# Kernel optimization log

Measured on AMD Instinct MI355X. Metric: run time of the kernel, lower is better.

The kernel has to match this reference:

```python
import jax, jax.numpy as jnp
import numpy as np

IN_F = 4096
OUT_F = 11008
FP_F = 256


def setup_inputs() -> dict:
    key = jax.random.key(0)
    ks = jax.random.split(key, 6)
    x = jax.random.normal(ks[0], (8, 64, IN_F), dtype=jnp.float32)
    # int8-valued quantized weight, stored as int32 for the harness
    q_weight = jax.random.randint(ks[1], (OUT_F, IN_F), -128, 128, dtype=jnp.int32)
    # per-output-column weight scale (like absmax/127), small positive
    scale_col = (jax.random.uniform(ks[2], (1, OUT_F), dtype=jnp.float32) * 0.01 + 1e-4)
    # fp16-precision outlier weight columns (kept fp32 here)
    weight_cache = jax.random.normal(ks[3], (OUT_F, FP_F), dtype=jnp.float32) * 0.02
    # outlier column indices into in_features
    ind = jnp.sort(jax.random.randint(ks[4], (FP_F,), 0, IN_F, dtype=jnp.int32))
    bias = jax.random.normal(ks[5], (OUT_F,), dtype=jnp.float32) * 0.01
    return {"x": x, "q_weight": q_weight, "scale_col": scale_col,
            "weight_cache": weight_cache, "ind": ind, "bias": bias}


def reference(x, q_weight, scale_col, weight_cache, ind, bias):
    # Flatten leading dims: (M, in_features)
    inputs = x.reshape(-1, x.shape[-1])
    # ExtractOutliersAndSetToZeros: gather outlier activation columns, zero them
    act_outliers = inputs[:, ind]                       # (M, fp)
    inputs_z = inputs.at[:, ind].set(0.0)               # (M, in)
    # FindRowScale: per-row absmax / 127, then symmetric int8 quantization
    x_scale = jnp.max(jnp.abs(inputs_z), axis=1, keepdims=True) / 127.0  # (M,1)
    x_scale = jnp.maximum(x_scale, jnp.float32(1e-8))
    q_x = jnp.clip(jnp.round(inputs_z / x_scale), -128.0, 127.0)          # int8 values
    # int8 GEMM (accumulate in fp32): (M,in) @ (in,out)
    y_int = q_x @ q_weight.T.astype(jnp.float32)
    # fp16 outlier GEMM: (M,fp) @ (fp,out)
    outliers_fp = act_outliers @ weight_cache.T
    # dequantize: row scale * col scale, add outlier contribution and bias
    y1 = y_int * x_scale * scale_col + outliers_fp + bias
    return y1.reshape(x.shape[:-1] + (q_weight.shape[0],))
```

## Files before the change

kernel.cpp:

```cpp
#include <hip/hip_runtime.h>
#include <hip/hip_fp16.h>

#define IN_F 4096
#define OUT_F 11008
#define FP_F 256
#define NROWS 512
#define BN 64

typedef int v4i __attribute__((ext_vector_type(4)));
typedef float v4f __attribute__((ext_vector_type(4)));
typedef _Float16 half8 __attribute__((ext_vector_type(8)));

__device__ __forceinline__ int pack4(v4i a) {
  return (int)((unsigned)(a[0] & 255) | ((unsigned)(a[1] & 255) << 8) |
               ((unsigned)(a[2] & 255) << 16) | ((unsigned)(a[3] & 255) << 24));
}

__global__ __launch_bounds__(256) void quant_kernel(
    const float* __restrict__ x, const int* __restrict__ ind,
    signed char* __restrict__ qx, _Float16* __restrict__ act,
    float* __restrict__ xscale)
{
  const int m = blockIdx.x;
  const int t = threadIdx.x;
  __shared__ unsigned char zm[IN_F];
  __shared__ float wmax[4];
  int* zmi = (int*)zm;
  #pragma unroll
  for (int i = 0; i < IN_F / 4 / 256; ++i) zmi[t + i * 256] = 0;
  __syncthreads();
  const int idx = ind[t];
  zm[idx] = 1;
  __syncthreads();

  const float* xr = x + (size_t)m * IN_F;
  float v[16];
  float amax = 0.f;
  const int k0 = t * 16;
  #pragma unroll
  for (int q = 0; q < 4; ++q) {
    v4f f = *(const v4f*)(xr + k0 + q * 4);
    #pragma unroll
    for (int j = 0; j < 4; ++j) {
      float mv = zm[k0 + q * 4 + j] ? 0.f : f[j];
      v[q * 4 + j] = mv;
      amax = fmaxf(amax, fabsf(mv));
    }
  }
  #pragma unroll
  for (int off = 32; off >= 1; off >>= 1)
    amax = fmaxf(amax, __shfl_xor(amax, off));
  if ((t & 63) == 0) wmax[t >> 6] = amax;
  __syncthreads();
  amax = fmaxf(fmaxf(wmax[0], wmax[1]), fmaxf(wmax[2], wmax[3]));
  const float scale = fmaxf(amax / 127.0f, 1e-8f);
  if (t == 0) xscale[m] = scale;
  const float inv = 1.0f / scale;

  union { signed char b[16]; v4i w4; } pk;
  #pragma unroll
  for (int j = 0; j < 16; ++j) {
    float qv = rintf(v[j] * inv);
    qv = fminf(fmaxf(qv, -128.f), 127.f);
    pk.b[j] = (signed char)qv;
  }
  const int mg = m >> 4;
  const int kb = t >> 2;
  const int lane = (m & 15) + 16 * (t & 3);
  ((v4i*)qx)[(mg * 64 + kb) * 64 + lane] = pk.w4;

  act[m * FP_F + t] = (_Float16)xr[idx];
}

__global__ __launch_bounds__(512) void gemm_kernel(
    const signed char* __restrict__ qx, const int* __restrict__ qw,
    const float* __restrict__ scol, const float* __restrict__ wc,
    const float* __restrict__ bias, const _Float16* __restrict__ act,
    const float* __restrict__ xscale, float* __restrict__ out)
{
  __shared__ __align__(16) signed char blds[2][4096];
  const int tid = threadIdx.x;
  const int w = tid >> 6;
  const int l = tid & 63;
  const int n0 = blockIdx.x * BN;

  const int c = tid >> 7;
  const int sl = (tid >> 1) & 63;
  const int h = tid & 1;
  const int brow = n0 + c * 16 + (sl & 15);
  const int* bsrc = qw + (size_t)brow * IN_F + ((sl >> 4) * 16 + h * 8);
  signed char* bdst = &blds[0][0] + (c * 1024 + sl * 16 + h * 8);

  v4i br[2][2];
  br[0][0] = *(const v4i*)(bsrc + 0);
  br[0][1] = *(const v4i*)(bsrc + 4);
  br[1][0] = *(const v4i*)(bsrc + 64);
  br[1][1] = *(const v4i*)(bsrc + 68);

  v4i acc[4][4] = {};

  {
    int2 d;
    d.x = pack4(br[0][0]);
    d.y = pack4(br[0][1]);
    *(int2*)(bdst) = d;
  }
  __syncthreads();

  const v4i* qx4 = (const v4i*)qx;
  const int aBase = (w * 4) * 4096 + l;

#define K_STEP(T, CUR) do {                                                   \
    const int t_ = (T);                                                       \
    v4i a[4];                                                                 \
    _Pragma("unroll")                                                         \
    for (int mf = 0; mf < 4; ++mf)                                            \
      a[mf] = qx4[aBase + mf * 4096 + t_ * 64];                               \
    if (t_ + 1 < 64) {                                                        \
      int2 d;                                                                 \
      d.x = pack4(br[(CUR) ^ 1][0]);                                          \
      d.y = pack4(br[(CUR) ^ 1][1]);                                          \
      *(int2*)(bdst + ((CUR) ^ 1) * 4096) = d;                                \
    }                                                                         \
    if (t_ + 2 < 64) {                                                        \
      const int* s_ = bsrc + (t_ + 2) * 64;                                   \
      br[CUR][0] = *(const v4i*)(s_);                                         \
      br[CUR][1] = *(const v4i*)(s_ + 4);                                     \
    }                                                                         \
    const signed char* rb = &blds[CUR][0];                                    \
    v4i b[4];                                                                 \
    _Pragma("unroll")                                                         \
    for (int nf = 0; nf < 4; ++nf)                                            \
      b[nf] = *(const v4i*)(rb + nf * 1024 + l * 16);                         \
    _Pragma("unroll")                                                         \
    for (int mf = 0; mf < 4; ++mf)                                            \
      _Pragma("unroll")                                                       \
      for (int nf = 0; nf < 4; ++nf)                                          \
        acc[mf][nf] = __builtin_amdgcn_mfma_i32_16x16x64_i8(                  \
            a[mf], b[nf], acc[mf][nf], 0, 0, 0);                              \
    __syncthreads();                                                          \
  } while (0)

  for (int t2 = 0; t2 < 64; t2 += 2) {
    K_STEP(t2, 0);
    K_STEP(t2 + 1, 1);
  }
#undef K_STEP

  float sc[4], bs[4];
  #pragma unroll
  for (int nf = 0; nf < 4; ++nf) {
    sc[nf] = scol[n0 + nf * 16 + (l & 15)];
    bs[nf] = bias[n0 + nf * 16 + (l & 15)];
  }
  float xs[4][4];
  #pragma unroll
  for (int mf = 0; mf < 4; ++mf)
    #pragma unroll
    for (int j = 0; j < 4; ++j)
      xs[mf][j] = xscale[w * 64 + mf * 16 + (l >> 4) * 4 + j];

  v4f facc[4][4];
  #pragma unroll
  for (int mf = 0; mf < 4; ++mf)
    #pragma unroll
    for (int nf = 0; nf < 4; ++nf)
      #pragma unroll
      for (int j = 0; j < 4; ++j)
        facc[mf][nf][j] = (float)acc[mf][nf][j] * xs[mf][j] * sc[nf];

  #pragma unroll
  for (int ks = 0; ks < 8; ++ks) {
    const int kk = ks * 32 + (l >> 4) * 8;
    half8 ah[4];
    #pragma unroll
    for (int mf = 0; mf < 4; ++mf) {
      const int row = w * 64 + mf * 16 + (l & 15);
      ah[mf] = *(const half8*)(act + row * FP_F + kk);
    }
    half8 bh[4];
    #pragma unroll
    for (int nf = 0; nf < 4; ++nf) {
      const float* wr = wc + (size_t)(n0 + nf * 16 + (l & 15)) * FP_F + kk;
      v4f w0 = *(const v4f*)(wr);
      v4f w1 = *(const v4f*)(wr + 4);
      half8 hb;
      #pragma unroll
      for (int j = 0; j < 4; ++j) {
        hb[j] = (_Float16)w0[j];
        hb[4 + j] = (_Float16)w1[j];
      }
      bh[nf] = hb;
    }
    #pragma unroll
    for (int mf = 0; mf < 4; ++mf)
      #pragma unroll
      for (int nf = 0; nf < 4; ++nf)
        facc[mf][nf] = __builtin_amdgcn_mfma_f32_16x16x32_f16(
            ah[mf], bh[nf], facc[mf][nf], 0, 0, 0);
  }

  #pragma unroll
  for (int mf = 0; mf < 4; ++mf)
    #pragma unroll
    for (int nf = 0; nf < 4; ++nf) {
      const int col = n0 + nf * 16 + (l & 15);
      #pragma unroll
      for (int j = 0; j < 4; ++j) {
        const int row = w * 64 + mf * 16 + (l >> 4) * 4 + j;
        out[(size_t)row * OUT_F + col] = facc[mf][nf][j] + bs[nf];
      }
    }
}

extern "C" void kernel_launch(void* const* d_in, const int* in_sizes, int n_in,
                              void* d_out, int out_size, void* d_ws, size_t ws_size,
                              hipStream_t stream) {
  const float* x      = (const float*)d_in[0];
  const int*   qw     = (const int*)d_in[1];
  const float* scol   = (const float*)d_in[2];
  const float* wcache = (const float*)d_in[3];
  const int*   ind    = (const int*)d_in[4];
  const float* bias   = (const float*)d_in[5];
  float* out = (float*)d_out;

  signed char* qx = (signed char*)d_ws;
  _Float16* act = (_Float16*)((char*)d_ws + (size_t)NROWS * IN_F);
  float* xscale = (float*)((char*)d_ws + (size_t)NROWS * IN_F + (size_t)NROWS * FP_F * 2);

  quant_kernel<<<NROWS, 256, 0, stream>>>(x, ind, qx, act, xscale);
  gemm_kernel<<<OUT_F / BN, 512, 0, stream>>>(qx, qw, scol, wcache, bias, act, xscale, out);
}
```

Measured before the change: 88.33 us.

## Split GEMM into smaller N tiles and two M halves, drop LDS staging

Halves the N tile width and splits the 512 rows across two blocks, quadrupling the grid so more compute units are busy. Weight tiles are now loaded straight from global memory into registers and packed per lane, instead of being double-buffered through shared memory with per-step barriers. In exchange, each weight row is fetched by two blocks, relying on L2 sharing. Per-lane weight loads are also less coalesced than the previous cooperative staging.

```diff
diff --git a/kernel.cpp b/kernel.cpp
--- a/kernel.cpp
+++ b/kernel.cpp
@@ -5,7 +5,8 @@
 #define OUT_F 11008
 #define FP_F 256
 #define NROWS 512
-#define BN 64
+#define BN 32
+#define NTILES (OUT_F / BN)
 
 typedef int v4i __attribute__((ext_vector_type(4)));
 typedef float v4f __attribute__((ext_vector_type(4)));
@@ -72,84 +73,58 @@
   act[m * FP_F + t] = (_Float16)xr[idx];
 }
 
-__global__ __launch_bounds__(512) void gemm_kernel(
+__global__ __launch_bounds__(256) void gemm_kernel(
     const signed char* __restrict__ qx, const int* __restrict__ qw,
     const float* __restrict__ scol, const float* __restrict__ wc,
     const float* __restrict__ bias, const _Float16* __restrict__ act,
     const float* __restrict__ xscale, float* __restrict__ out)
 {
-  __shared__ __align__(16) signed char blds[2][4096];
   const int tid = threadIdx.x;
   const int w = tid >> 6;
   const int l = tid & 63;
-  const int n0 = blockIdx.x * BN;
-
-  const int c = tid >> 7;
-  const int sl = (tid >> 1) & 63;
-  const int h = tid & 1;
-  const int brow = n0 + c * 16 + (sl & 15);
-  const int* bsrc = qw + (size_t)brow * IN_F + ((sl >> 4) * 16 + h * 8);
-  signed char* bdst = &blds[0][0] + (c * 1024 + sl * 16 + h * 8);
-
-  v4i br[2][2];
-  br[0][0] = *(const v4i*)(bsrc + 0);
-  br[0][1] = *(const v4i*)(bsrc + 4);
-  br[1][0] = *(const v4i*)(bsrc + 64);
-  br[1][1] = *(const v4i*)(bsrc + 68);
-
-  v4i acc[4][4] = {};
-
-  {
-    int2 d;
-    d.x = pack4(br[0][0]);
-    d.y = pack4(br[0][1]);
-    *(int2*)(bdst) = d;
-  }
-  __syncthreads();
+  const int mtile = blockIdx.x & 1;
+  const int ntile = blockIdx.x >> 1;
+  const int n0 = ntile * BN;
+  const int row0 = mtile * 256 + w * 64;
 
   const v4i* qx4 = (const v4i*)qx;
-  const int aBase = (w * 4) * 4096 + l;
-
-#define K_STEP(T, CUR) do {                                                   \
-    const int t_ = (T);                                                       \
-    v4i a[4];                                                                 \
-    _Pragma("unroll")                                                         \
-    for (int mf = 0; mf < 4; ++mf)                                            \
-      a[mf] = qx4[aBase + mf * 4096 + t_ * 64];                               \
-    if (t_ + 1 < 64) {                                                        \
-      int2 d;                                                                 \
-      d.x = pack4(br[(CUR) ^ 1][0]);                                          \
-      d.y = pack4(br[(CUR) ^ 1][1]);                                          \
-      *(int2*)(bdst + ((CUR) ^ 1) * 4096) = d;                                \
-    }                                                                         \
-    if (t_ + 2 < 64) {                                                        \
-      const int* s_ = bsrc + (t_ + 2) * 64;                                   \
-      br[CUR][0] = *(const v4i*)(s_);                                         \
-      br[CUR][1] = *(const v4i*)(s_ + 4);                                     \
-    }                                                                         \
-    const signed char* rb = &blds[CUR][0];                                    \
-    v4i b[4];                                                                 \
-    _Pragma("unroll")                                                         \
-    for (int nf = 0; nf < 4; ++nf)                                            \
-      b[nf] = *(const v4i*)(rb + nf * 1024 + l * 16);                         \
-    _Pragma("unroll")                                                         \
-    for (int mf = 0; mf < 4; ++mf)                                            \
-      _Pragma("unroll")                                                       \
-      for (int nf = 0; nf < 4; ++nf)                                          \
-        acc[mf][nf] = __builtin_amdgcn_mfma_i32_16x16x64_i8(                  \
-            a[mf], b[nf], acc[mf][nf], 0, 0, 0);                              \
-    __syncthreads();                                                          \
-  } while (0)
-
-  for (int t2 = 0; t2 < 64; t2 += 2) {
-    K_STEP(t2, 0);
-    K_STEP(t2 + 1, 1);
-  }
-#undef K_STEP
-
-  float sc[4], bs[4];
-  #pragma unroll
-  for (int nf = 0; nf < 4; ++nf) {
+  const int aBase = (row0 >> 4) * 4096 + l;
+  const int* qwb = qw + (size_t)(n0 + (l & 15)) * IN_F + ((l >> 4) << 4);
+
+  v4i acc[4][2] = {};
+
+  #pragma unroll 2
+  for (int kb = 0; kb < 64; ++kb) {
+    v4i a[4];
+    #pragma unroll
+    for (int mf = 0; mf < 4; ++mf)
+      a[mf] = qx4[aBase + mf * 4096 + kb * 64];
+    v4i b[2];
+    #pragma unroll
+    for (int nf = 0; nf < 2; ++nf) {
+      const int* s = qwb + nf * 16 * IN_F + kb * 64;
+      v4i r0 = *(const v4i*)(s);
+      v4i r1 = *(const v4i*)(s + 4);
+      v4i r2 = *(const v4i*)(s + 8);
+      v4i r3 = *(const v4i*)(s + 12);
+      v4i pb;
+      pb[0] = pack4(r0);
+      pb[1] = pack4(r1);
+      pb[2] = pack4(r2);
+      pb[3] = pack4(r3);
+      b[nf] = pb;
+    }
+    #pragma unroll
+    for (int mf = 0; mf < 4; ++mf)
+      #pragma unroll
+      for (int nf = 0; nf < 2; ++nf)
+        acc[mf][nf] = __builtin_amdgcn_mfma_i32_16x16x64_i8(
+            a[mf], b[nf], acc[mf][nf], 0, 0, 0);
+  }
+
+  float sc[2], bs[2];
+  #pragma unroll
+  for (int nf = 0; nf < 2; ++nf) {
     sc[nf] = scol[n0 + nf * 16 + (l & 15)];
     bs[nf] = bias[n0 + nf * 16 + (l & 15)];
   }
@@ -158,13 +133,13 @@
   for (int mf = 0; mf < 4; ++mf)
     #pragma unroll
     for (int j = 0; j < 4; ++j)
-      xs[mf][j] = xscale[w * 64 + mf * 16 + (l >> 4) * 4 + j];
-
-  v4f facc[4][4];
+      xs[mf][j] = xscale[row0 + mf * 16 + (l >> 4) * 4 + j];
+
+  v4f facc[4][2];
   #pragma unroll
   for (int mf = 0; mf < 4; ++mf)
     #pragma unroll
-    for (int nf = 0; nf < 4; ++nf)
+    for (int nf = 0; nf < 2; ++nf)
       #pragma unroll
       for (int j = 0; j < 4; ++j)
         facc[mf][nf][j] = (float)acc[mf][nf][j] * xs[mf][j] * sc[nf];
@@ -175,12 +150,12 @@
     half8 ah[4];
     #pragma unroll
     for (int mf = 0; mf < 4; ++mf) {
-      const int row = w * 64 + mf * 16 + (l & 15);
+      const int row = row0 + mf * 16 + (l & 15);
       ah[mf] = *(const half8*)(act + row * FP_F + kk);
     }
-    half8 bh[4];
-    #pragma unroll
-    for (int nf = 0; nf < 4; ++nf) {
+    half8 bh[2];
+    #pragma unroll
+    for (int nf = 0; nf < 2; ++nf) {
       const float* wr = wc + (size_t)(n0 + nf * 16 + (l & 15)) * FP_F + kk;
       v4f w0 = *(const v4f*)(wr);
       v4f w1 = *(const v4f*)(wr + 4);
@@ -195,7 +170,7 @@
     #pragma unroll
     for (int mf = 0; mf < 4; ++mf)
       #pragma unroll
-      for (int nf = 0; nf < 4; ++nf)
+      for (int nf = 0; nf < 2; ++nf)
         facc[mf][nf] = __builtin_amdgcn_mfma_f32_16x16x32_f16(
             ah[mf], bh[nf], facc[mf][nf], 0, 0, 0);
   }
@@ -203,11 +178,11 @@
   #pragma unroll
   for (int mf = 0; mf < 4; ++mf)
     #pragma unroll
-    for (int nf = 0; nf < 4; ++nf) {
+    for (int nf = 0; nf < 2; ++nf) {
       const int col = n0 + nf * 16 + (l & 15);
       #pragma unroll
       for (int j = 0; j < 4; ++j) {
-        const int row = w * 64 + mf * 16 + (l >> 4) * 4 + j;
+        const int row = row0 + mf * 16 + (l >> 4) * 4 + j;
         out[(size_t)row * OUT_F + col] = facc[mf][nf][j] + bs[nf];
       }
     }
@@ -229,5 +204,5 @@
   float* xscale = (float*)((char*)d_ws + (size_t)NROWS * IN_F + (size_t)NROWS * FP_F * 2);
 
   quant_kernel<<<NROWS, 256, 0, stream>>>(x, ind, qx, act, xscale);
-  gemm_kernel<<<OUT_F / BN, 512, 0, stream>>>(qx, qw, scol, wcache, bias, act, xscale, out);
-}
+  gemm_kernel<<<NTILES * 2, 256, 0, stream>>>(qx, qw, scol, wcache, bias, act, xscale, out);
+}
```

New measurement: 228.2 us. +158.4%, slower.
